# Optimization experiments

Measured on AMD Instinct MI355X. Metric: run time of the kernel, lower is better.

The kernel has to match this reference:

```python
import jax, jax.numpy as jnp
import numpy as np

B, T, V, H = 1, 1024, 32000, 2048
NH, NKV, HD = 8, 4, 256
QS, KVS = NH * HD, NKV * HD
I, L = 8192, 2
SCALE = 256.0 ** -0.5          # query_pre_attn_scalar ** -0.5
ATTN_CAP, FINAL_CAP = 50.0, 30.0
WIN, EPS, THETA = 512, 1e-6, 10000.0
NEG = -2.3819763e38


def setup_inputs() -> dict:
    key = jax.random.key(0)
    ks = jax.random.split(key, 12)
    s = 0.02
    return {
        "tokens": jax.random.randint(ks[0], (B, T), 0, V, dtype=jnp.int32),
        "embed": jax.random.normal(ks[1], (V, H), jnp.float32) * s,
        "qkv_w": jax.random.normal(ks[2], (L, (NH + 2 * NKV) * HD, H), jnp.float32) * s,
        "o_w": jax.random.normal(ks[3], (L, H, NH * HD), jnp.float32) * s,
        "gate_w": jax.random.normal(ks[4], (L, I, H), jnp.float32) * s,
        "up_w": jax.random.normal(ks[5], (L, I, H), jnp.float32) * s,
        "down_w": jax.random.normal(ks[6], (L, H, I), jnp.float32) * s,
        "ln_in": jax.random.normal(ks[7], (L, H), jnp.float32) * s,   # RMSNorm weight (zeros-init offset)
        "ln_pa": jax.random.normal(ks[8], (L, H), jnp.float32) * s,
        "ln_pre": jax.random.normal(ks[9], (L, H), jnp.float32) * s,
        "ln_post": jax.random.normal(ks[10], (L, H), jnp.float32) * s,
        "ln_f": jax.random.normal(ks[11], (H,), jnp.float32) * s,
    }


def rmsnorm(x, w):
    x = x.astype(jnp.float32)
    n = x * jax.lax.rsqrt(jnp.mean(x * x, axis=-1, keepdims=True) + EPS)
    return n * (1.0 + w)  # add_unit_offset=True


def rope(x, cos, sin):
    # x: [B, T, N, HD]; split-half complex rotary as in apply_rotary_emb
    x1, x2 = jnp.split(x, 2, axis=-1)
    c = cos[None, :, None, :]
    s = sin[None, :, None, :]
    return jnp.concatenate([x1 * c - x2 * s, x1 * s + x2 * c], axis=-1)


def reference(tokens, embed, qkv_w, o_w, gate_w, up_w, down_w,
              ln_in, ln_pa, ln_pre, ln_post, ln_f):
    pos = jnp.arange(T)
    inv = 1.0 / (THETA ** (jnp.arange(0, HD, 2, dtype=jnp.float32) / HD))  # [HD/2]
    ang = pos.astype(jnp.float32)[:, None] * inv[None, :]
    cos, sin = jnp.cos(ang), jnp.sin(ang)

    i, j = pos[:, None], pos[None, :]
    causal = j <= i
    mask_global = jnp.where(causal, 0.0, NEG).astype(jnp.float32)
    mask_local = jnp.where(causal & (i - j < WIN), 0.0, NEG).astype(jnp.float32)
    masks = [mask_local, mask_global]  # layer 0: LOCAL_SLIDING, layer 1: GLOBAL

    x = embed[tokens] * jnp.sqrt(jnp.float32(H))  # Gemma embedding normalizer

    for l in range(L):
        h = rmsnorm(x, ln_in[l])
        qkv = jnp.einsum('bth,oh->bto', h, qkv_w[l])
        q = qkv[..., :QS].reshape(B, T, NH, HD)
        k = qkv[..., QS:QS + KVS].reshape(B, T, NKV, HD)
        v = qkv[..., QS + KVS:].reshape(B, T, NKV, HD)
        q = rope(q, cos, sin)
        k = rope(k, cos, sin)
        # prefill: kv_write_indices=arange(T) -> cache == current k/v
        k = jnp.repeat(k, NH // NKV, axis=2)  # GQA repeat_interleave over heads
        v = jnp.repeat(v, NH // NKV, axis=2)
        scores = jnp.einsum('bqhd,bkhd->bhqk', q * SCALE, k)
        scores = jnp.tanh(scores / ATTN_CAP) * ATTN_CAP
        scores = scores + masks[l][None, None]
        attn = jax.nn.softmax(scores.astype(jnp.float32), axis=-1)
        out = jnp.einsum('bhqk,bkhd->bqhd', attn, v).reshape(B, T, NH * HD)
        out = jnp.einsum('bto,ho->bth', out, o_w[l])
        x = x + rmsnorm(out, ln_pa[l])

        h = rmsnorm(x, ln_pre[l])
        gate = jax.nn.gelu(jnp.einsum('bth,ih->bti', h, gate_w[l]), approximate=True)
        up = jnp.einsum('bth,ih->bti', h, up_w[l])
        ff = jnp.einsum('bti,hi->bth', gate * up, down_w[l])
        x = x + rmsnorm(ff, ln_post[l])

    x = rmsnorm(x, ln_f)
    logits = jnp.einsum('bth,vh->btv', x, embed)
    logits = jnp.tanh(logits / FINAL_CAP) * FINAL_CAP  # final_logit_softcapping
    return logits
```

## Files before the change

kernel.cpp:

```cpp
#include <hip/hip_runtime.h>
#include <hip/hip_bf16.h>
#include <math.h>

typedef unsigned short u16;
typedef __attribute__((ext_vector_type(8))) short bf16x8;
typedef __attribute__((ext_vector_type(4))) float f32x4;
typedef __attribute__((ext_vector_type(4))) u16 u16x4;

#define T_SEQ 1024
#define HDIM  2048
#define NHEAD 8
#define NKVH  4
#define HSZ   256
#define ISZ   8192
#define NVOC  32000

#define GLDS(src, dst) __builtin_amdgcn_global_load_lds( \
    (const __attribute__((address_space(1))) void*)(src), \
    (__attribute__((address_space(3))) void*)(dst), 16, 0, 0)

__device__ __forceinline__ u16 f2bf(float f) {
    union { float f; unsigned u; } v; v.f = f;
    return (u16)((v.u + 0x7fffu + ((v.u >> 16) & 1u)) >> 16);
}
__device__ __forceinline__ float bf2f(u16 h) {
    union { unsigned u; float f; } v; v.u = (unsigned)h << 16; return v.f;
}

__device__ __forceinline__ float fast_tanh(float x) {
    float e = __expf(-2.0f * fabsf(x));
    float t = (1.0f - e) / (1.0f + e);
    return copysignf(t, x);
}

__device__ __forceinline__ f32x4 mfma16(bf16x8 a, bf16x8 b, f32x4 c) {
    return __builtin_amdgcn_mfma_f32_16x16x32_bf16(a, b, c, 0, 0, 0);
}

__global__ __launch_bounds__(256)
void cvt_bf16(const float* __restrict__ s, u16* __restrict__ d, long n4)
{
    for (long i = blockIdx.x * 256L + threadIdx.x; i < n4; i += (long)gridDim.x * 256) {
        f32x4 v = ((const f32x4*)s)[i];
        u16x4 o;
        o.x = f2bf(v.x); o.y = f2bf(v.y); o.z = f2bf(v.z); o.w = f2bf(v.w);
        ((u16x4*)d)[i] = o;
    }
}

template<int EPI>
__global__ __launch_bounds__(512, 1)
void gemm_dp(const u16* __restrict__ A, int lda,
             const u16* __restrict__ B, int ldb,
             float* __restrict__ C, int ldc, long sC, int K)
{
    extern __shared__ u16 lds[];
    const int t = threadIdx.x;
    const int lane = t & 63, wid = t >> 6;
    const int z = blockIdx.z;
    A += (long)z * K;
    B += (long)z * K;
    C += (long)z * sC;

    const int nwg = gridDim.x * gridDim.y;
    int flat = blockIdx.y * gridDim.x + blockIdx.x;
    {
        const int q = nwg >> 3, r = nwg & 7;
        const int xcd = flat & 7, loc = flat >> 3;
        flat = (xcd < r ? xcd * (q + 1) : r * (q + 1) + (xcd - r) * q) + loc;
    }
    const int gm = gridDim.y;
    const long m0 = (long)(flat % gm) * 128;
    const long n0 = (long)(flat / gm) * 256;

    const int sr = t >> 3;
    const int sl = ((t & 7) ^ (sr & 7)) * 8;
    const u16* gA0 = A + (m0 + sr)       * (long)lda + sl;
    const u16* gA1 = A + (m0 + 64 + sr)  * (long)lda + sl;
    const u16* gB0 = B + (n0 + sr)       * (long)ldb + sl;
    const u16* gB1 = B + (n0 + 64 + sr)  * (long)ldb + sl;
    const u16* gB2 = B + (n0 + 128 + sr) * (long)ldb + sl;
    const u16* gB3 = B + (n0 + 192 + sr) * (long)ldb + sl;

    auto stage = [&](int kt) {
        const long ko = (long)kt * 64;
        char* d = (char*)lds + (kt % 3) * 49152 + t * 16;
        GLDS(gA0 + ko, d);
        GLDS(gA1 + ko, d + 8192);
        GLDS(gB0 + ko, d + 16384);
        GLDS(gB1 + ko, d + 24576);
        GLDS(gB2 + ko, d + 32768);
        GLDS(gB3 + ko, d + 40960);
    };

    f32x4 acc[4][4] = {};
    const int fr = lane & 15, kq = lane >> 4;
    const int wm = wid >> 2, wn = wid & 3;
    const int ps0 = ((kq)     ^ (lane & 7)) * 8;
    const int ps1 = ((4 + kq) ^ (lane & 7)) * 8;

    const int KT = K >> 6;
    stage(0);
    if (KT > 1) stage(1);
    if (KT > 2) stage(2);

    for (int kt = 0; kt < KT; ++kt) {
        if (kt < KT - 2)       asm volatile("s_waitcnt vmcnt(12)" ::: "memory");
        else if (kt == KT - 2) asm volatile("s_waitcnt vmcnt(6)" ::: "memory");
        else                   asm volatile("s_waitcnt vmcnt(0)" ::: "memory");
        __builtin_amdgcn_s_barrier();

        const u16* Asl = lds + (kt % 3) * 24576;
        const u16* Bsl = Asl + 8192;
        #pragma unroll
        for (int kk = 0; kk < 2; ++kk) {
            const int ps = kk ? ps1 : ps0;
            bf16x8 af[4], bfv[4];
            #pragma unroll
            for (int mi = 0; mi < 4; ++mi)
                af[mi] = *(const bf16x8*)(Asl + (wm * 64 + mi * 16 + fr) * 64 + ps);
            #pragma unroll
            for (int ni = 0; ni < 4; ++ni)
                bfv[ni] = *(const bf16x8*)(Bsl + (wn * 64 + ni * 16 + fr) * 64 + ps);
            #pragma unroll
            for (int mi = 0; mi < 4; ++mi)
                #pragma unroll
                for (int ni = 0; ni < 4; ++ni)
                    acc[mi][ni] = mfma16(af[mi], bfv[ni], acc[mi][ni]);
        }
        __builtin_amdgcn_s_barrier();
        if (kt + 3 < KT) stage(kt + 3);
    }

    const int crb = kq * 4, ccol = fr;
    #pragma unroll
    for (int mi = 0; mi < 4; ++mi) {
        #pragma unroll
        for (int rr = 0; rr < 4; ++rr) {
            const long row = m0 + wm * 64 + mi * 16 + crb + rr;
            float* cp = C + row * ldc + n0 + wn * 64 + ccol;
            #pragma unroll
            for (int ni = 0; ni < 4; ++ni) {
                float v = acc[mi][ni][rr];
                if (EPI == 1) v = fast_tanh(v * (1.0f / 30.0f)) * 30.0f;
                cp[ni * 16] = v;
            }
        }
    }
}

template<int EPI>
__global__ __launch_bounds__(512, 1)
void gemm8(const u16* __restrict__ A, int lda,
           const u16* __restrict__ B, int ldb,
           float* __restrict__ C, int ldc, long sC, int K)
{
    extern __shared__ u16 lds[];
    const int t = threadIdx.x;
    const int lane = t & 63, wid = t >> 6;
    const int z = blockIdx.z;
    A += (long)z * K;
    B += (long)z * K;
    C += (long)z * sC;

    const int nwg = gridDim.x * gridDim.y;
    int flat = blockIdx.y * gridDim.x + blockIdx.x;
    {
        const int q = nwg >> 3, r = nwg & 7;
        const int xcd = flat & 7, loc = flat >> 3;
        flat = (xcd < r ? xcd * (q + 1) : r * (q + 1) + (xcd - r) * q) + loc;
    }
    const int gm = gridDim.y;
    const long m0 = (long)(flat % gm) * 256;
    const long n0 = (long)(flat / gm) * 256;

    const int sr = t >> 3;
    const int sl = ((t & 7) ^ (sr & 7)) * 8;
    const u16* gA = A + (m0 + sr) * (long)lda + sl;
    const u16* gB = B + (n0 + sr) * (long)ldb + sl;

    auto stA = [&](int kt, int ro) {
        char* d = (char*)lds + (kt & 1) * 65536 + ro * 128 + t * 16;
        GLDS(gA + (long)ro * lda + (long)kt * 64, d);
    };
    auto stB = [&](int kt, int ro) {
        char* d = (char*)lds + (kt & 1) * 65536 + 32768 + ro * 128 + t * 16;
        GLDS(gB + (long)ro * ldb + (long)kt * 64, d);
    };

    f32x4 acc[8][4] = {};
    const int fr = lane & 15, kq = lane >> 4;
    const int wm = wid >> 2, wn = wid & 3;
    const int g0 = ((kq) ^ (lane & 7)) * 8;
    const int g1 = ((4 + kq) ^ (lane & 7)) * 8;
    const int KT = K >> 6;

    stA(0, 0); stA(0, 64); stA(0, 128); stA(0, 192);
    stB(0, 0); stB(0, 64); stB(0, 128); stB(0, 192);
    stA(1, 0); stA(1, 64); stA(1, 128); stA(1, 192);
    stB(1, 0); stB(1, 64); stB(1, 128); stB(1, 192);
    asm volatile("s_waitcnt vmcnt(8)" ::: "memory");
    __builtin_amdgcn_s_barrier();

    for (int kt = 0; kt < KT; ++kt) {
        const u16* As = lds + (kt & 1) * 32768;
        const u16* Bs = As + 16384;
        const int arow = wm * 128 + fr;
        const int brow = wn * 64 + fr;
        bf16x8 aL[4][2], aH[4][2], bL[2][2], bH[2][2];

        #pragma unroll
        for (int mi = 0; mi < 4; ++mi) {
            aL[mi][0] = *(const bf16x8*)(As + (arow + mi * 16) * 64 + g0);
            aL[mi][1] = *(const bf16x8*)(As + (arow + mi * 16) * 64 + g1);
        }
        #pragma unroll
        for (int ni = 0; ni < 2; ++ni) {
            bL[ni][0] = *(const bf16x8*)(Bs + (brow + ni * 16) * 64 + g0);
            bL[ni][1] = *(const bf16x8*)(Bs + (brow + ni * 16) * 64 + g1);
        }
        __builtin_amdgcn_s_barrier();
        asm volatile("s_waitcnt lgkmcnt(0)" ::: "memory");
        __builtin_amdgcn_sched_barrier(0);
        __builtin_amdgcn_s_setprio(1);
        #pragma unroll
        for (int mi = 0; mi < 4; ++mi)
            #pragma unroll
            for (int ni = 0; ni < 2; ++ni) {
                acc[mi][ni] = mfma16(aL[mi][0], bL[ni][0], acc[mi][ni]);
                acc[mi][ni] = mfma16(aL[mi][1], bL[ni][1], acc[mi][ni]);
            }
        __builtin_amdgcn_s_setprio(0);
        __builtin_amdgcn_s_barrier();

        #pragma unroll
        for (int ni = 0; ni < 2; ++ni) {
            bH[ni][0] = *(const bf16x8*)(Bs + (brow + (ni + 2) * 16) * 64 + g0);
            bH[ni][1] = *(const bf16x8*)(Bs + (brow + (ni + 2) * 16) * 64 + g1);
        }
        __builtin_amdgcn_s_barrier();
        asm volatile("s_waitcnt lgkmcnt(0)" ::: "memory");
        __builtin_amdgcn_sched_barrier(0);
        __builtin_amdgcn_s_setprio(1);
        #pragma unroll
        for (int mi = 0; mi < 4; ++mi)
            #pragma unroll
            for (int ni = 0; ni < 2; ++ni) {
                acc[mi][ni + 2] = mfma16(aL[mi][0], bH[ni][0], acc[mi][ni + 2]);
                acc[mi][ni + 2] = mfma16(aL[mi][1], bH[ni][1], acc[mi][ni + 2]);
            }
        __builtin_amdgcn_s_setprio(0);
        __builtin_amdgcn_s_barrier();

        #pragma unroll
        for (int mi = 0; mi < 4; ++mi) {
            aH[mi][0] = *(const bf16x8*)(As + (arow + (mi + 4) * 16) * 64 + g0);
            aH[mi][1] = *(const bf16x8*)(As + (arow + (mi + 4) * 16) * 64 + g1);
        }
        if (kt + 2 < KT) { stB(kt + 2, 0); stB(kt + 2, 64); stB(kt + 2, 128); stB(kt + 2, 192); }
        __builtin_amdgcn_s_barrier();
        asm volatile("s_waitcnt lgkmcnt(0)" ::: "memory");
        __builtin_amdgcn_sched_barrier(0);
        __builtin_amdgcn_s_setprio(1);
        #pragma unroll
        for (int mi = 0; mi < 4; ++mi)
            #pragma unroll
            for (int ni = 0; ni < 2; ++ni) {
                acc[mi + 4][ni] = mfma16(aH[mi][0], bL[ni][0], acc[mi + 4][ni]);
                acc[mi + 4][ni] = mfma16(aH[mi][1], bL[ni][1], acc[mi + 4][ni]);
            }
        __builtin_amdgcn_s_setprio(0);
        __builtin_amdgcn_s_barrier();

        if (kt + 2 < KT) { stA(kt + 2, 0); stA(kt + 2, 64); stA(kt + 2, 128); stA(kt + 2, 192); }
        __builtin_amdgcn_s_barrier();
        __builtin_amdgcn_sched_barrier(0);
        __builtin_amdgcn_s_setprio(1);
        #pragma unroll
        for (int mi = 0; mi < 4; ++mi)
            #pragma unroll
            for (int ni = 0; ni < 2; ++ni) {
                acc[mi + 4][ni + 2] = mfma16(aH[mi][0], bH[ni][0], acc[mi + 4][ni + 2]);
                acc[mi + 4][ni + 2] = mfma16(aH[mi][1], bH[ni][1], acc[mi + 4][ni + 2]);
            }
        __builtin_amdgcn_s_setprio(0);
        if (kt + 1 < KT) {
            if (kt + 2 < KT) asm volatile("s_waitcnt vmcnt(8)" ::: "memory");
            else             asm volatile("s_waitcnt vmcnt(0)" ::: "memory");
            __builtin_amdgcn_s_barrier();
        }
    }

    const int crb = kq * 4, ccol = fr;
    #pragma unroll
    for (int mj = 0; mj < 8; ++mj) {
        #pragma unroll
        for (int rr = 0; rr < 4; ++rr) {
            const long row = m0 + wm * 128 + mj * 16 + crb + rr;
            float* cp = C + row * ldc + n0 + wn * 64 + ccol;
            #pragma unroll
            for (int ni = 0; ni < 4; ++ni) {
                float v = acc[mj][ni][rr];
                if (EPI == 1) v = fast_tanh(v * (1.0f / 30.0f)) * 30.0f;
                cp[ni * 16] = v;
            }
        }
    }
}

template<int EPI, typename CT>
__global__ __launch_bounds__(256)
void gemm_bt(const u16* __restrict__ A, int lda, long sA,
             const u16* __restrict__ B, int ldb, long sB, int bshift,
             CT* __restrict__ C, int ldc, long sC, int K)
{
    __shared__ u16 As[128 * 32];
    __shared__ u16 Bs[128 * 32];
    const int tid = threadIdx.x;
    const int lane = tid & 63, wid = tid >> 6;
    const int z = blockIdx.z;
    A += (long)z * sA;
    B += (long)(z >> bshift) * sB;
    C += (long)z * sC;

    const int nwg = gridDim.x * gridDim.y;
    int flat = blockIdx.y * gridDim.x + blockIdx.x;
    {
        const int q = nwg >> 3, r = nwg & 7;
        const int xcd = flat & 7, loc = flat >> 3;
        flat = (xcd < r ? xcd * (q + 1) : r * (q + 1) + (xcd - r) * q) + loc;
    }
    const int gm = gridDim.y;
    const long m0 = (long)(flat % gm) * 128;
    const long n0 = (long)(flat / gm) * 128;

    f32x4 acc[4][4] = {};

    const int ar = tid >> 2, ac = (tid & 3) * 8;
    const u16* gA0 = A + (m0 + ar) * lda + ac;
    const u16* gB0 = B + (n0 + ar) * (long)ldb + ac;
    const long a64 = 64L * lda, b64 = 64L * ldb;

    const int fr = lane & 15, fk = (lane >> 4) * 8;
    const int wm = (wid >> 1) * 64, wn = (wid & 1) * 64;

    for (int k0 = 0; k0 < K; k0 += 32) {
        GLDS(gA0 + k0,       &As[tid * 8]);
        GLDS(gA0 + a64 + k0, &As[2048 + tid * 8]);
        GLDS(gB0 + k0,       &Bs[tid * 8]);
        GLDS(gB0 + b64 + k0, &Bs[2048 + tid * 8]);
        __syncthreads();
        bf16x8 af[4], bfv[4];
        #pragma unroll
        for (int mi = 0; mi < 4; ++mi)
            af[mi] = *(const bf16x8*)(&As[(wm + mi * 16 + fr) * 32 + fk]);
        #pragma unroll
        for (int ni = 0; ni < 4; ++ni)
            bfv[ni] = *(const bf16x8*)(&Bs[(wn + ni * 16 + fr) * 32 + fk]);
        #pragma unroll
        for (int mi = 0; mi < 4; ++mi)
            #pragma unroll
            for (int ni = 0; ni < 4; ++ni)
                acc[mi][ni] = mfma16(af[mi], bfv[ni], acc[mi][ni]);
        __syncthreads();
    }

    const int crb = (lane >> 4) * 4, ccol = lane & 15;
    #pragma unroll
    for (int mi = 0; mi < 4; ++mi) {
        #pragma unroll
        for (int rr = 0; rr < 4; ++rr) {
            const long row = m0 + wm + mi * 16 + crb + rr;
            CT* cp = C + row * ldc + n0 + wn + ccol;
            #pragma unroll
            for (int ni = 0; ni < 4; ++ni) {
                float v = acc[mi][ni][rr];
                if (EPI == 1) v = fast_tanh(v * (1.0f / 30.0f)) * 30.0f;
                if constexpr (sizeof(CT) == 2) cp[ni * 16] = f2bf(v);
                else                           cp[ni * 16] = v;
            }
        }
    }
}

__global__ __launch_bounds__(256)
void embed_scale(const int* __restrict__ tok, const float* __restrict__ emb,
                 float* __restrict__ x)
{
    const int t = blockIdx.x, tid = threadIdx.x;
    const long src = (long)tok[t] * HDIM;
    f32x4 a = *(const f32x4*)(emb + src + tid * 8);
    f32x4 b = *(const f32x4*)(emb + src + tid * 8 + 4);
    a *= 45.254834f; b *= 45.254834f;
    *(f32x4*)(x + (long)t * HDIM + tid * 8) = a;
    *(f32x4*)(x + (long)t * HDIM + tid * 8 + 4) = b;
}

__device__ __forceinline__ float block_sum(float v, float* red) {
    #pragma unroll
    for (int o = 32; o; o >>= 1) v += __shfl_xor(v, o);
    const int tid = threadIdx.x;
    if ((tid & 63) == 0) red[tid >> 6] = v;
    __syncthreads();
    return red[0] + red[1] + red[2] + red[3];
}

__global__ __launch_bounds__(256)
void rmsnorm_bf16(const float* __restrict__ x, const float* __restrict__ w,
                  u16* __restrict__ out)
{
    __shared__ float red[4];
    const int t = blockIdx.x, tid = threadIdx.x;
    const float* row = x + (long)t * HDIM;
    f32x4 a = *(const f32x4*)(row + tid * 8);
    f32x4 b = *(const f32x4*)(row + tid * 8 + 4);
    float ss = a.x*a.x + a.y*a.y + a.z*a.z + a.w*a.w
             + b.x*b.x + b.y*b.y + b.z*b.z + b.w*b.w;
    ss = block_sum(ss, red);
    const float r = rsqrtf(ss * (1.0f / HDIM) + 1e-6f);
    f32x4 wa = *(const f32x4*)(w + tid * 8);
    f32x4 wb = *(const f32x4*)(w + tid * 8 + 4);
    u16x4 o0, o1;
    o0.x = f2bf(a.x * r * (1.0f + wa.x)); o0.y = f2bf(a.y * r * (1.0f + wa.y));
    o0.z = f2bf(a.z * r * (1.0f + wa.z)); o0.w = f2bf(a.w * r * (1.0f + wa.w));
    o1.x = f2bf(b.x * r * (1.0f + wb.x)); o1.y = f2bf(b.y * r * (1.0f + wb.y));
    o1.z = f2bf(b.z * r * (1.0f + wb.z)); o1.w = f2bf(b.w * r * (1.0f + wb.w));
    *(u16x4*)(out + (long)t * HDIM + tid * 8) = o0;
    *(u16x4*)(out + (long)t * HDIM + tid * 8 + 4) = o1;
}

__global__ __launch_bounds__(256)
void add_rmsnorm(float* __restrict__ x, const float* __restrict__ y,
                 const float* __restrict__ w, int nsplit, long stride)
{
    __shared__ float red[4];
    const int t = blockIdx.x, tid = threadIdx.x;
    const float* yr = y + (long)t * HDIM;
    f32x4 a = *(const f32x4*)(yr + tid * 8);
    f32x4 b = *(const f32x4*)(yr + tid * 8 + 4);
    for (int s = 1; s < nsplit; ++s) {
        a += *(const f32x4*)(yr + s * stride + tid * 8);
        b += *(const f32x4*)(yr + s * stride + tid * 8 + 4);
    }
    float ss = a.x*a.x + a.y*a.y + a.z*a.z + a.w*a.w
             + b.x*b.x + b.y*b.y + b.z*b.z + b.w*b.w;
    ss = block_sum(ss, red);
    const float r = rsqrtf(ss * (1.0f / HDIM) + 1e-6f);
    f32x4 wa = *(const f32x4*)(w + tid * 8);
    f32x4 wb = *(const f32x4*)(w + tid * 8 + 4);
    float* xr = x + (long)t * HDIM;
    f32x4 xa = *(const f32x4*)(xr + tid * 8);
    f32x4 xb = *(const f32x4*)(xr + tid * 8 + 4);
    xa.x += a.x * r * (1.0f + wa.x); xa.y += a.y * r * (1.0f + wa.y);
    xa.z += a.z * r * (1.0f + wa.z); xa.w += a.w * r * (1.0f + wa.w);
    xb.x += b.x * r * (1.0f + wb.x); xb.y += b.y * r * (1.0f + wb.y);
    xb.z += b.z * r * (1.0f + wb.z); xb.w += b.w * r * (1.0f + wb.w);
    *(f32x4*)(xr + tid * 8) = xa;
    *(f32x4*)(xr + tid * 8 + 4) = xb;
}

#define QKV_STRIDE (1024L * 4096)

__global__ __launch_bounds__(256)
void qkv_post(const float* __restrict__ qkv, u16* __restrict__ qb,
              u16* __restrict__ kb)
{
    const int t = blockIdx.x, tid = threadIdx.x;
    const float* row = qkv + (long)t * 4096;
    const float ft = (float)t;
    #pragma unroll
    for (int it = 0; it < 4; ++it) {
        const int p = tid + it * 256;
        const int nh = p >> 7, d = p & 127;
        const float inv = powf(10000.0f, -(float)d * (1.0f / 128.0f));
        const float ang = ft * inv;
        const float c = cosf(ang), s = sinf(ang);
        const int i1 = nh * 256 + d, i2 = i1 + 128;
        const float x1 = row[i1] + row[i1 + QKV_STRIDE];
        const float x2 = row[i2] + row[i2 + QKV_STRIDE];
        const long ob = ((long)nh * T_SEQ + t) * HSZ;
        qb[ob + d]       = f2bf((x1 * c - x2 * s) * 0.0625f);
        qb[ob + 128 + d] = f2bf((x1 * s + x2 * c) * 0.0625f);
    }
    #pragma unroll
    for (int it = 0; it < 2; ++it) {
        const int p = tid + it * 256;
        const int kv = p >> 7, d = p & 127;
        const float inv = powf(10000.0f, -(float)d * (1.0f / 128.0f));
        const float ang = ft * inv;
        const float c = cosf(ang), s = sinf(ang);
        const int i1 = 2048 + kv * 256 + d, i2 = i1 + 128;
        const float x1 = row[i1] + row[i1 + QKV_STRIDE];
        const float x2 = row[i2] + row[i2 + QKV_STRIDE];
        const long ob = ((long)kv * T_SEQ + t) * HSZ;
        kb[ob + d]       = f2bf(x1 * c - x2 * s);
        kb[ob + 128 + d] = f2bf(x1 * s + x2 * c);
    }
}

__global__ __launch_bounds__(256)
void v_transpose(const float* __restrict__ qkvb, u16* __restrict__ vT)
{
    __shared__ u16 tile[64][65];
    const int t0 = blockIdx.x * 64, d0 = blockIdx.y * 64, kv = blockIdx.z;
    const int lane = threadIdx.x & 63, w = threadIdx.x >> 6;
    #pragma unroll
    for (int i = 0; i < 16; ++i) {
        const int t = w * 16 + i;
        const long idx = (long)(t0 + t) * 4096 + 3072 + kv * 256 + d0 + lane;
        tile[t][lane] = f2bf(qkvb[idx] + qkvb[idx + QKV_STRIDE]);
    }
    __syncthreads();
    #pragma unroll
    for (int i = 0; i < 16; ++i) {
        const int d = w * 16 + i;
        vT[((long)kv * HSZ + d0 + d) * T_SEQ + t0 + lane] = tile[lane][d];
    }
}

__global__ __launch_bounds__(256)
void softmax_mask(const float* __restrict__ sc, u16* __restrict__ pr, int win)
{
    __shared__ float redm[4], reds[4];
    const int i = blockIdx.x, h = blockIdx.y, tid = threadIdx.x;
    const long base = ((long)h * T_SEQ + i) * T_SEQ;
    f32x4 sv = *(const f32x4*)(sc + base + tid * 4);
    float vals[4];
    #pragma unroll
    for (int j = 0; j < 4; ++j) {
        const int col = tid * 4 + j;
        const float s = fast_tanh(sv[j] * 0.02f) * 50.0f;
        const bool valid = (col <= i) && ((i - col) < win);
        vals[j] = valid ? s : -3.0e38f;
    }
    float m = fmaxf(fmaxf(vals[0], vals[1]), fmaxf(vals[2], vals[3]));
    #pragma unroll
    for (int o = 32; o; o >>= 1) m = fmaxf(m, __shfl_xor(m, o));
    if ((tid & 63) == 0) redm[tid >> 6] = m;
    __syncthreads();
    m = fmaxf(fmaxf(redm[0], redm[1]), fmaxf(redm[2], redm[3]));
    float sum = 0.0f;
    #pragma unroll
    for (int j = 0; j < 4; ++j) { vals[j] = __expf(vals[j] - m); sum += vals[j]; }
    #pragma unroll
    for (int o = 32; o; o >>= 1) sum += __shfl_xor(sum, o);
    if ((tid & 63) == 0) reds[tid >> 6] = sum;
    __syncthreads();
    sum = reds[0] + reds[1] + reds[2] + reds[3];
    const float inv = 1.0f / sum;
    u16x4 o4;
    #pragma unroll
    for (int j = 0; j < 4; ++j) o4[j] = f2bf(vals[j] * inv);
    *(u16x4*)(pr + base + tid * 4) = o4;
}

__global__ __launch_bounds__(256)
void mul_gelu(const float* __restrict__ g, const float* __restrict__ u,
              u16* __restrict__ p)
{
    const int n4 = (T_SEQ * ISZ) / 4;
    for (int i = blockIdx.x * 256 + threadIdx.x; i < n4; i += gridDim.x * 256) {
        f32x4 gv = ((const f32x4*)g)[i];
        f32x4 uv = ((const f32x4*)u)[i];
        u16x4 w;
        #pragma unroll
        for (int j = 0; j < 4; ++j) {
            const float xg = gv[j];
            const float tt = fast_tanh(0.79788456f * (xg + 0.044715f * xg * xg * xg));
            w[j] = f2bf(0.5f * xg * (1.0f + tt) * uv[j]);
        }
        ((u16x4*)p)[i] = w;
    }
}

extern "C" void kernel_launch(void* const* d_in, const int* in_sizes, int n_in,
                              void* d_out, int out_size, void* d_ws, size_t ws_size,
                              hipStream_t stream)
{
    (void)in_sizes; (void)n_in; (void)out_size; (void)ws_size;
    const int*   tokens = (const int*)  d_in[0];
    const float* emb    = (const float*)d_in[1];
    const float* qkv_w  = (const float*)d_in[2];
    const float* o_w    = (const float*)d_in[3];
    const float* gate_w = (const float*)d_in[4];
    const float* up_w   = (const float*)d_in[5];
    const float* down_w = (const float*)d_in[6];
    const float* ln_in  = (const float*)d_in[7];
    const float* ln_pa  = (const float*)d_in[8];
    const float* ln_pre = (const float*)d_in[9];
    const float* ln_post= (const float*)d_in[10];
    const float* ln_f   = (const float*)d_in[11];
    float* logits = (float*)d_out;

    char* base = (char*)d_ws;
    size_t off = 0;
    auto alloc = [&](size_t b) { char* p = base + off; off += (b + 255) & ~(size_t)255; return p; };

    float* x    = (float*)alloc((size_t)T_SEQ * HDIM * 4);
    u16*   hb   = (u16*)  alloc((size_t)T_SEQ * HDIM * 2);
    u16*   qb   = (u16*)  alloc((size_t)NHEAD * T_SEQ * HSZ * 2);
    u16*   kb   = (u16*)  alloc((size_t)NKVH * T_SEQ * HSZ * 2);
    u16*   vT   = (u16*)  alloc((size_t)NKVH * HSZ * T_SEQ * 2);
    u16*   ao   = (u16*)  alloc((size_t)T_SEQ * HDIM * 2);
    u16*   pb   = (u16*)  alloc((size_t)T_SEQ * ISZ * 2);
    char*  big  = alloc((size_t)2 * T_SEQ * ISZ * 4);
    float* P    = (float*)big;
    float* sc   = (float*)big;
    u16*   pr   = (u16*)(big + (size_t)NHEAD * T_SEQ * T_SEQ * 4);
    float* gb   = (float*)big;
    float* ub   = (float*)(big + (size_t)T_SEQ * ISZ * 4);
    u16*   wb   = (u16*)  alloc((size_t)NVOC * HDIM * 2);

    const size_t LDSD = 3 * 49152;
    const size_t LDS8 = 2 * 65536;
    const long s2048 = 1024L * 2048;

    embed_scale<<<T_SEQ, 256, 0, stream>>>(tokens, emb, x);
    for (int l = 0; l < 2; ++l) {
        rmsnorm_bf16<<<T_SEQ, 256, 0, stream>>>(x, ln_in + l * HDIM, hb);
        cvt_bf16<<<2048, 256, 0, stream>>>(qkv_w + (size_t)l * 4096 * HDIM, wb, 4096L * HDIM / 4);
        gemm_dp<0><<<dim3(16, 8, 2), 512, LDSD, stream>>>(
            hb, HDIM, wb, HDIM, P, 4096, QKV_STRIDE, 1024);
        qkv_post<<<T_SEQ, 256, 0, stream>>>(P, qb, kb);
        v_transpose<<<dim3(16, 4, 4), 256, 0, stream>>>(P, vT);
        gemm_bt<0, float><<<dim3(8, 8, NHEAD), 256, 0, stream>>>(
            qb, HSZ, (long)T_SEQ * HSZ, kb, HSZ, (long)T_SEQ * HSZ, 1,
            sc, T_SEQ, (long)T_SEQ * T_SEQ, HSZ);
        softmax_mask<<<dim3(T_SEQ, NHEAD, 1), 256, 0, stream>>>(
            sc, pr, l == 0 ? 512 : (1 << 30));
        gemm_bt<0, u16><<<dim3(2, 8, NHEAD), 256, 0, stream>>>(
            pr, T_SEQ, (long)T_SEQ * T_SEQ, vT, T_SEQ, (long)HSZ * T_SEQ, 1,
            ao, HDIM, (long)HSZ, T_SEQ);
        cvt_bf16<<<2048, 256, 0, stream>>>(o_w + (size_t)l * HDIM * HDIM, wb, (long)HDIM * HDIM / 4);
        gemm_dp<0><<<dim3(8, 8, 4), 512, LDSD, stream>>>(
            ao, HDIM, wb, HDIM, P, HDIM, s2048, 512);
        add_rmsnorm<<<T_SEQ, 256, 0, stream>>>(x, P, ln_pa + l * HDIM, 4, s2048);
        rmsnorm_bf16<<<T_SEQ, 256, 0, stream>>>(x, ln_pre + l * HDIM, hb);
        cvt_bf16<<<2048, 256, 0, stream>>>(gate_w + (size_t)l * ISZ * HDIM, wb, (long)ISZ * HDIM / 4);
        gemm_dp<0><<<dim3(32, 8, 1), 512, LDSD, stream>>>(
            hb, HDIM, wb, HDIM, gb, ISZ, 0, HDIM);
        cvt_bf16<<<2048, 256, 0, stream>>>(up_w + (size_t)l * ISZ * HDIM, wb, (long)ISZ * HDIM / 4);
        gemm_dp<0><<<dim3(32, 8, 1), 512, LDSD, stream>>>(
            hb, HDIM, wb, HDIM, ub, ISZ, 0, HDIM);
        mul_gelu<<<2048, 256, 0, stream>>>(gb, ub, pb);
        cvt_bf16<<<2048, 256, 0, stream>>>(down_w + (size_t)l * HDIM * ISZ, wb, (long)HDIM * ISZ / 4);
        gemm_dp<0><<<dim3(8, 8, 4), 512, LDSD, stream>>>(
            pb, ISZ, wb, ISZ, P, HDIM, s2048, 2048);
        add_rmsnorm<<<T_SEQ, 256, 0, stream>>>(x, P, ln_post + l * HDIM, 4, s2048);
    }
    rmsnorm_bf16<<<T_SEQ, 256, 0, stream>>>(x, ln_f, hb);
    cvt_bf16<<<2048, 256, 0, stream>>>(emb, wb, (long)NVOC * HDIM / 4);
    gemm8<1><<<dim3(125, 4, 1), 512, LDS8, stream>>>(
        hb, HDIM, wb, HDIM, logits, NVOC, 0, HDIM);
}
```

Measured before the change: 888.5 us.

## Skip masked attention tiles and trim barriers in the pipelined GEMM loop

The score GEMM now returns early for 128x128 tiles that lie entirely above the causal diagonal or outside the sliding window. The probability-times-V GEMM limits its K loop to the causal and window range of each row block. Together these cut attention FLOPs and memory traffic. Separately, the main GEMM loop drops several intermediate s_barrier, waitcnt and sched_barrier calls and issues the B-tile prefetch earlier, to cut synchronisation stalls between MFMA phases. The risks are LDS hazards once the explicit waits are gone, and softmax reading score tiles that were never written (it relies on masking them out).

```diff
diff --git a/kernel.cpp b/kernel.cpp
--- a/kernel.cpp
+++ b/kernel.cpp
@@ -219,9 +219,6 @@
             bL[ni][0] = *(const bf16x8*)(Bs + (brow + ni * 16) * 64 + g0);
             bL[ni][1] = *(const bf16x8*)(Bs + (brow + ni * 16) * 64 + g1);
         }
-        __builtin_amdgcn_s_barrier();
-        asm volatile("s_waitcnt lgkmcnt(0)" ::: "memory");
-        __builtin_amdgcn_sched_barrier(0);
         __builtin_amdgcn_s_setprio(1);
         #pragma unroll
         for (int mi = 0; mi < 4; ++mi)
@@ -231,16 +228,12 @@
                 acc[mi][ni] = mfma16(aL[mi][1], bL[ni][1], acc[mi][ni]);
             }
         __builtin_amdgcn_s_setprio(0);
-        __builtin_amdgcn_s_barrier();
 
         #pragma unroll
         for (int ni = 0; ni < 2; ++ni) {
             bH[ni][0] = *(const bf16x8*)(Bs + (brow + (ni + 2) * 16) * 64 + g0);
             bH[ni][1] = *(const bf16x8*)(Bs + (brow + (ni + 2) * 16) * 64 + g1);
         }
-        __builtin_amdgcn_s_barrier();
-        asm volatile("s_waitcnt lgkmcnt(0)" ::: "memory");
-        __builtin_amdgcn_sched_barrier(0);
         __builtin_amdgcn_s_setprio(1);
         #pragma unroll
         for (int mi = 0; mi < 4; ++mi)
@@ -252,15 +245,12 @@
         __builtin_amdgcn_s_setprio(0);
         __builtin_amdgcn_s_barrier();
 
+        if (kt + 2 < KT) { stB(kt + 2, 0); stB(kt + 2, 64); stB(kt + 2, 128); stB(kt + 2, 192); }
         #pragma unroll
         for (int mi = 0; mi < 4; ++mi) {
             aH[mi][0] = *(const bf16x8*)(As + (arow + (mi + 4) * 16) * 64 + g0);
             aH[mi][1] = *(const bf16x8*)(As + (arow + (mi + 4) * 16) * 64 + g1);
         }
-        if (kt + 2 < KT) { stB(kt + 2, 0); stB(kt + 2, 64); stB(kt + 2, 128); stB(kt + 2, 192); }
-        __builtin_amdgcn_s_barrier();
-        asm volatile("s_waitcnt lgkmcnt(0)" ::: "memory");
-        __builtin_amdgcn_sched_barrier(0);
         __builtin_amdgcn_s_setprio(1);
         #pragma unroll
         for (int mi = 0; mi < 4; ++mi)
@@ -273,8 +263,6 @@
         __builtin_amdgcn_s_barrier();
 
         if (kt + 2 < KT) { stA(kt + 2, 0); stA(kt + 2, 64); stA(kt + 2, 128); stA(kt + 2, 192); }
-        __builtin_amdgcn_s_barrier();
-        __builtin_amdgcn_sched_barrier(0);
         __builtin_amdgcn_s_setprio(1);
         #pragma unroll
         for (int mi = 0; mi < 4; ++mi)
@@ -312,7 +300,8 @@
 __global__ __launch_bounds__(256)
 void gemm_bt(const u16* __restrict__ A, int lda, long sA,
              const u16* __restrict__ B, int ldb, long sB, int bshift,
-             CT* __restrict__ C, int ldc, long sC, int K)
+             CT* __restrict__ C, int ldc, long sC, int K,
+             int swin, int tflag)
 {
     __shared__ u16 As[128 * 32];
     __shared__ u16 Bs[128 * 32];
@@ -334,6 +323,18 @@
     const long m0 = (long)(flat % gm) * 128;
     const long n0 = (long)(flat / gm) * 128;
 
+    if (swin > 0) {
+        if (n0 > m0 + 127) return;
+        if (m0 - (n0 + 127) >= swin) return;
+    }
+    int klo = 0, khi = K;
+    if (tflag > 0) {
+        const long hi = m0 + 128;
+        if (hi < khi) khi = (int)hi;
+        const long lo = m0 - (long)tflag + 1;
+        klo = lo > 0 ? (int)(lo & ~31L) : 0;
+    }
+
     f32x4 acc[4][4] = {};
 
     const int ar = tid >> 2, ac = (tid & 3) * 8;
@@ -344,7 +345,7 @@
     const int fr = lane & 15, fk = (lane >> 4) * 8;
     const int wm = (wid >> 1) * 64, wn = (wid & 1) * 64;
 
-    for (int k0 = 0; k0 < K; k0 += 32) {
+    for (int k0 = klo; k0 < khi; k0 += 32) {
         GLDS(gA0 + k0,       &As[tid * 8]);
         GLDS(gA0 + a64 + k0, &As[2048 + tid * 8]);
         GLDS(gB0 + k0,       &Bs[tid * 8]);
@@ -614,9 +615,11 @@
     const size_t LDSD = 3 * 49152;
     const size_t LDS8 = 2 * 65536;
     const long s2048 = 1024L * 2048;
+    const int BIGWIN = 1 << 29;
 
     embed_scale<<<T_SEQ, 256, 0, stream>>>(tokens, emb, x);
     for (int l = 0; l < 2; ++l) {
+        const int win = (l == 0) ? 512 : BIGWIN;
         rmsnorm_bf16<<<T_SEQ, 256, 0, stream>>>(x, ln_in + l * HDIM, hb);
         cvt_bf16<<<2048, 256, 0, stream>>>(qkv_w + (size_t)l * 4096 * HDIM, wb, 4096L * HDIM / 4);
         gemm_dp<0><<<dim3(16, 8, 2), 512, LDSD, stream>>>(
@@ -625,12 +628,12 @@
         v_transpose<<<dim3(16, 4, 4), 256, 0, stream>>>(P, vT);
         gemm_bt<0, float><<<dim3(8, 8, NHEAD), 256, 0, stream>>>(
             qb, HSZ, (long)T_SEQ * HSZ, kb, HSZ, (long)T_SEQ * HSZ, 1,
-            sc, T_SEQ, (long)T_SEQ * T_SEQ, HSZ);
+            sc, T_SEQ, (long)T_SEQ * T_SEQ, HSZ, win, 0);
         softmax_mask<<<dim3(T_SEQ, NHEAD, 1), 256, 0, stream>>>(
             sc, pr, l == 0 ? 512 : (1 << 30));
         gemm_bt<0, u16><<<dim3(2, 8, NHEAD), 256, 0, stream>>>(
             pr, T_SEQ, (long)T_SEQ * T_SEQ, vT, T_SEQ, (long)HSZ * T_SEQ, 1,
-            ao, HDIM, (long)HSZ, T_SEQ);
+            ao, HDIM, (long)HSZ, T_SEQ, 0, win);
         cvt_bf16<<<2048, 256, 0, stream>>>(o_w + (size_t)l * HDIM * HDIM, wb, (long)HDIM * HDIM / 4);
         gemm_dp<0><<<dim3(8, 8, 4), 512, LDSD, stream>>>(
             ao, HDIM, wb, HDIM, P, HDIM, s2048, 512);
```

Result: no change. 875.6 us (-1.5%).
